# Kernel tuning notes

Measured on AMD Instinct MI355X. Metric: run time of the kernel, lower is better.

Reference implementation:

```python
import jax, jax.numpy as jnp
import numpy as np

D = 1024      # hidden_dim
E = 8         # num_experts
F = 512       # expert_dim


def setup_inputs() -> dict:
    key = jax.random.key(0)
    ks = jax.random.split(key, 7)
    B, N = 4, 4096
    s1 = 1.0 / np.sqrt(D)
    s2 = 1.0 / np.sqrt(F)
    return {
        "x": jax.random.normal(ks[0], (B, N, D), dtype=jnp.float32),
        "W1": jax.random.uniform(ks[1], (E, D, F), jnp.float32, -s1, s1),  # per-expert first linear
        "b1": jax.random.uniform(ks[2], (E, F), jnp.float32, -s1, s1),
        "W2": jax.random.uniform(ks[3], (E, F, D), jnp.float32, -s2, s2),  # per-expert second linear
        "b2": jax.random.uniform(ks[4], (E, D), jnp.float32, -s2, s2),
        "Wr": jax.random.uniform(ks[5], (D, E), jnp.float32, -s1, s1),    # router
        "br": jax.random.uniform(ks[6], (E,), jnp.float32, -s1, s1),
    }


def reference(x, W1, b1, W2, b2, Wr, br):
    # Router: softmax over experts per token. [B,N,E]
    router_weights = jax.nn.softmax(x @ Wr + br, axis=-1)
    # All experts on all tokens (dense soft-MoE), batched as grouped GEMMs.
    h = jax.nn.gelu(jnp.einsum('bnd,edf->bnef', x, W1) + b1, approximate=False)  # [B,N,E,F]
    y = jnp.einsum('bnef,efd->bned', h, W2) + b2[None, None]                      # [B,N,E,D]
    # Softmax-weighted combine over experts.
    return jnp.einsum('bned,bne->bnd', y, router_weights)
```

## Files before the change

### kernel.cpp

```cpp
#include <hip/hip_runtime.h>
#include <hip/hip_bf16.h>
#include <math.h>

#define MTOK 16384
#define DDIM 1024
#define EEXP 8
#define FDIM 512
#define EFK  4096

typedef __attribute__((ext_vector_type(8))) short short8;
typedef __attribute__((ext_vector_type(4))) float floatx4;

__device__ __forceinline__ void gld_lds16(const void* g, void* l) {
  __builtin_amdgcn_global_load_lds((const __attribute__((address_space(1))) void*)g,
                                   (__attribute__((address_space(3))) void*)l, 16, 0, 0);
}

__device__ __forceinline__ float gelu_fast(float v) {
  const float z  = v * 0.70710678118654752f;
  const float az = fabsf(z);
  const float t  = __builtin_amdgcn_rcpf(1.f + 0.3275911f * az);
  const float poly = t * (0.254829592f +
                     t * (-0.284496736f +
                     t * (1.421413741f +
                     t * (-1.453152027f +
                     t * 1.061405429f))));
  const float ex = __expf(-az * az);
  float erfv = 1.f - poly * ex;
  erfv = copysignf(erfv, z);
  return 0.5f * v * (1.f + erfv);
}

__global__ __launch_bounds__(256) void transpose_cast_kernel(
    const float* __restrict__ in, __hip_bfloat16* __restrict__ out, int R, int C) {
  __shared__ float tile[32][33];
  const float* inb = in + (size_t)blockIdx.z * R * C;
  __hip_bfloat16* outb = out + (size_t)blockIdx.z * R * C;
  const int c0 = blockIdx.x * 32, r0 = blockIdx.y * 32;
  const int tx = threadIdx.x & 31, ty = threadIdx.x >> 5;
#pragma unroll
  for (int i = 0; i < 4; ++i)
    tile[ty + i * 8][tx] = inb[(size_t)(r0 + ty + i * 8) * C + (c0 + tx)];
  __syncthreads();
#pragma unroll
  for (int i = 0; i < 4; ++i)
    outb[(size_t)(c0 + ty + i * 8) * R + (r0 + tx)] = __float2bfloat16(tile[tx][ty + i * 8]);
}

__global__ __launch_bounds__(256) void router_cast_kernel(
    const float* __restrict__ x, const float* __restrict__ Wr, const float* __restrict__ br,
    __hip_bfloat16* __restrict__ xbf, float* __restrict__ r) {
  const int wave = (blockIdx.x * 256 + threadIdx.x) >> 6;
  const int lane = threadIdx.x & 63;
  const float* xr = x + (size_t)wave * DDIM;
  float acc[EEXP];
#pragma unroll
  for (int e = 0; e < EEXP; ++e) acc[e] = 0.f;
#pragma unroll
  for (int i = 0; i < DDIM / 64; ++i) {
    const int d = i * 64 + lane;
    const float xv = xr[d];
    xbf[(size_t)wave * DDIM + d] = __float2bfloat16(xv);
    const float4* w4 = (const float4*)(Wr + (size_t)d * EEXP);
    const float4 w0 = w4[0], w1 = w4[1];
    acc[0] += xv * w0.x; acc[1] += xv * w0.y; acc[2] += xv * w0.z; acc[3] += xv * w0.w;
    acc[4] += xv * w1.x; acc[5] += xv * w1.y; acc[6] += xv * w1.z; acc[7] += xv * w1.w;
  }
#pragma unroll
  for (int off = 32; off; off >>= 1) {
#pragma unroll
    for (int e = 0; e < EEXP; ++e) acc[e] += __shfl_xor(acc[e], off, 64);
  }
  float mx = -1e30f;
#pragma unroll
  for (int e = 0; e < EEXP; ++e) { acc[e] += br[e]; mx = fmaxf(mx, acc[e]); }
  float s = 0.f;
#pragma unroll
  for (int e = 0; e < EEXP; ++e) { acc[e] = expf(acc[e] - mx); s += acc[e]; }
  const float inv = 1.f / s;
  if (lane < EEXP) r[(size_t)wave * EEXP + lane] = acc[lane] * inv;
}

#define BUFSZ 65536
#define AOFF  0
#define BOFF  32768

#define STAGE_A(Q1, QM, K0)                                                        \
  do {                                                                             \
    _Pragma("unroll") for (int r_ = 0; r_ < 2; ++r_) {                             \
      gld_lds16(gA + (size_t)(r_ * 128 + (QM) * 64 + wid * 8 + l3) * LDA_ +        \
                    (K0) + ((l7 ^ l3) * 8),                                        \
                ldsb + (Q1) * BUFSZ + AOFF + (QM) * 16384 +                        \
                    (r_ * 64 + wid * 8) * 128);                                    \
    }                                                                              \
  } while (0)

#define STAGE_B(Q1, QN, K0)                                                        \
  do {                                                                             \
    _Pragma("unroll") for (int r_ = 0; r_ < 2; ++r_) {                             \
      const int lin_ = r_ * 64 + wid * 8 + l3;                                     \
      gld_lds16(gB + (size_t)((lin_ >> 5) * 64 + (QN) * 32 + (lin_ & 31)) * LDB_ + \
                    (K0) + ((l7 ^ l3) * 8),                                        \
                ldsb + (Q1) * BUFSZ + BOFF + (QN) * 16384 +                        \
                    (r_ * 64 + wid * 8) * 128);                                    \
    }                                                                              \
  } while (0)

#define PHASE(P, QM, QN, VM, LA, LB, STAGE_STMT)                                   \
  do {                                                                             \
    asm volatile("s_waitcnt vmcnt(" VM ")\n\ts_barrier" ::: "memory");             \
    if (LA) {                                                                      \
      _Pragma("unroll") for (int i_ = 0; i_ < 4; ++i_)                             \
        _Pragma("unroll") for (int k_ = 0; k_ < 2; ++k_)                           \
          af[i_][k_] = *(const short8*)(ldsb + (P) * BUFSZ + AOFF +                \
              (QM) * 16384 + (wr * 64 + i_ * 16 + lanem) * 128 +                   \
              (((k_ * 4 + laneq) ^ swz) * 16));                                    \
    }                                                                              \
    if (LB) {                                                                      \
      _Pragma("unroll") for (int j_ = 0; j_ < 2; ++j_)                             \
        _Pragma("unroll") for (int k_ = 0; k_ < 2; ++k_)                           \
          bf[j_][k_] = *(const short8*)(ldsb + (P) * BUFSZ + BOFF +                \
              (QN) * 16384 + (wc * 32 + j_ * 16 + lanem) * 128 +                   \
              (((k_ * 4 + laneq) ^ swz) * 16));                                    \
    }                                                                              \
    STAGE_STMT;                                                                    \
    __builtin_amdgcn_s_setprio(1);                                                 \
    _Pragma("unroll") for (int i_ = 0; i_ < 4; ++i_)                               \
      _Pragma("unroll") for (int j_ = 0; j_ < 2; ++j_)                             \
        _Pragma("unroll") for (int k_ = 0; k_ < 2; ++k_)                           \
          acc[(QM) * 4 + i_][(QN) * 2 + j_] =                                      \
              __builtin_amdgcn_mfma_f32_16x16x32_bf16(                             \
                  af[i_][k_], bf[j_][k_], acc[(QM) * 4 + i_][(QN) * 2 + j_],       \
                  0, 0, 0);                                                        \
    __builtin_amdgcn_s_setprio(0);                                                 \
  } while (0)

#define GEMM_CORE(NT)                                                              \
  STAGE_A(0, 0, 0);                                                                \
  STAGE_B(0, 0, 0);                                                                \
  STAGE_B(0, 1, 0);                                                                \
  STAGE_A(0, 1, 0);                                                                \
  for (int kt = 0; kt < (NT) - 1; ++kt) {                                          \
    const int p_ = kt & 1, q_ = p_ ^ 1, k1_ = (kt + 1) * 64;                       \
    PHASE(p_, 0, 0, "4", 1, 1, STAGE_A(q_, 0, k1_));                               \
    PHASE(p_, 0, 1, "4", 0, 1, STAGE_B(q_, 0, k1_));                               \
    PHASE(p_, 1, 1, "4", 1, 0, STAGE_B(q_, 1, k1_));                               \
    PHASE(p_, 1, 0, "6", 0, 1, STAGE_A(q_, 1, k1_));                               \
  }                                                                                \
  {                                                                                \
    const int p_ = ((NT) - 1) & 1;                                                 \
    PHASE(p_, 0, 0, "4", 1, 1, (void)0);                                           \
    PHASE(p_, 0, 1, "2", 0, 1, (void)0);                                           \
    PHASE(p_, 1, 1, "0", 1, 0, (void)0);                                           \
    PHASE(p_, 1, 0, "0", 0, 1, (void)0);                                           \
  }

__global__ __launch_bounds__(512, 2) void gemm_h_kernel(
    const __hip_bfloat16* __restrict__ A, const __hip_bfloat16* __restrict__ W1t,
    const float* __restrict__ b1, const float* __restrict__ r,
    __hip_bfloat16* __restrict__ Hs) {
  const int bid = blockIdx.x;
  const int strip = bid & 63, fb = (bid >> 6) & 1, e = bid >> 7;
  const int T0 = strip * 256, F0 = fb * 256;

  __shared__ char ldsb[2 * BUFSZ];

  const int tid = threadIdx.x, lane = tid & 63, wid = tid >> 6;
  const int wr = wid >> 2, wc = wid & 3;
  const int lanem = lane & 15, laneq = lane >> 4;
  const int l3 = lane >> 3, l7 = lane & 7;
  const int swz = lanem & 7;
  const int LDA_ = DDIM, LDB_ = DDIM;

  const __hip_bfloat16* gA = W1t + (size_t)e * FDIM * DDIM + (size_t)F0 * DDIM;
  const __hip_bfloat16* gB = A + (size_t)T0 * DDIM;

  floatx4 acc[8][4];
#pragma unroll
  for (int i = 0; i < 8; ++i)
#pragma unroll
    for (int j = 0; j < 4; ++j) acc[i][j] = (floatx4){0.f, 0.f, 0.f, 0.f};
  short8 af[4][2], bf[2][2];

  GEMM_CORE(DDIM / 64);

#pragma unroll
  for (int nj = 0; nj < 4; ++nj) {
    const int tok = T0 + wc * 64 + nj * 16 + lanem;
    const float rv = r[(size_t)tok * EEXP + e];
#pragma unroll
    for (int mi = 0; mi < 8; ++mi) {
      const int f = F0 + wr * 128 + mi * 16 + laneq * 4;
      const float4 b4 = *(const float4*)(b1 + e * FDIM + f);
      union { ushort4 u; __hip_bfloat16 h[4]; } pk;
      pk.h[0] = __float2bfloat16(gelu_fast(acc[mi][nj][0] + b4.x) * rv);
      pk.h[1] = __float2bfloat16(gelu_fast(acc[mi][nj][1] + b4.y) * rv);
      pk.h[2] = __float2bfloat16(gelu_fast(acc[mi][nj][2] + b4.z) * rv);
      pk.h[3] = __float2bfloat16(gelu_fast(acc[mi][nj][3] + b4.w) * rv);
      *(ushort4*)(Hs + (size_t)tok * EFK + e * FDIM + f) = pk.u;
    }
  }
}

__global__ __launch_bounds__(512, 2) void gemm_out_kernel(
    const __hip_bfloat16* __restrict__ Hs, const __hip_bfloat16* __restrict__ W2t,
    const float* __restrict__ b2, const float* __restrict__ r,
    float* __restrict__ out) {
  const int bid = blockIdx.x;
  const int strip = (bid >> 5) * 8 + (bid & 7);
  const int dq = (bid >> 3) & 3;
  const int T0 = strip * 256, D0 = dq * 256;

  __shared__ char ldsb[2 * BUFSZ];

  const int tid = threadIdx.x, lane = tid & 63, wid = tid >> 6;
  const int wr = wid >> 2, wc = wid & 3;
  const int lanem = lane & 15, laneq = lane >> 4;
  const int l3 = lane >> 3, l7 = lane & 7;
  const int swz = lanem & 7;
  const int LDA_ = EFK, LDB_ = EFK;

  const __hip_bfloat16* gA = W2t + (size_t)D0 * EFK;
  const __hip_bfloat16* gB = Hs + (size_t)T0 * EFK;

  floatx4 acc[8][4];
#pragma unroll
  for (int i = 0; i < 8; ++i)
#pragma unroll
    for (int j = 0; j < 4; ++j) acc[i][j] = (floatx4){0.f, 0.f, 0.f, 0.f};
  short8 af[4][2], bf[2][2];

  GEMM_CORE(EFK / 64);

#pragma unroll
  for (int mi = 0; mi < 8; ++mi) {
    const int d0 = D0 + wr * 128 + mi * 16 + laneq * 4;
    float4 b2v[EEXP];
#pragma unroll
    for (int e = 0; e < EEXP; ++e) b2v[e] = *(const float4*)(b2 + e * DDIM + d0);
#pragma unroll
    for (int nj = 0; nj < 4; ++nj) {
      const int tok = T0 + wc * 64 + nj * 16 + lanem;
      const float4* r4 = (const float4*)(r + (size_t)tok * EEXP);
      const float4 r0 = r4[0], r1 = r4[1];
      const float rv[EEXP] = {r0.x, r0.y, r0.z, r0.w, r1.x, r1.y, r1.z, r1.w};
      float bx = 0.f, by = 0.f, bz = 0.f, bw = 0.f;
#pragma unroll
      for (int e = 0; e < EEXP; ++e) {
        bx += rv[e] * b2v[e].x; by += rv[e] * b2v[e].y;
        bz += rv[e] * b2v[e].z; bw += rv[e] * b2v[e].w;
      }
      float4 o;
      o.x = acc[mi][nj][0] + bx; o.y = acc[mi][nj][1] + by;
      o.z = acc[mi][nj][2] + bz; o.w = acc[mi][nj][3] + bw;
      *(float4*)(out + (size_t)tok * DDIM + d0) = o;
    }
  }
}

extern "C" void kernel_launch(void* const* d_in, const int* in_sizes, int n_in,
                              void* d_out, int out_size, void* d_ws, size_t ws_size,
                              hipStream_t stream) {
  const float* x  = (const float*)d_in[0];
  const float* W1 = (const float*)d_in[1];
  const float* b1 = (const float*)d_in[2];
  const float* W2 = (const float*)d_in[3];
  const float* b2 = (const float*)d_in[4];
  const float* Wr = (const float*)d_in[5];
  const float* br = (const float*)d_in[6];
  float* out = (float*)d_out;

  char* ws = (char*)d_ws;
  __hip_bfloat16* xbf = (__hip_bfloat16*)(ws);
  __hip_bfloat16* W1t = (__hip_bfloat16*)(ws + (32u << 20));
  __hip_bfloat16* W2t = (__hip_bfloat16*)(ws + (40u << 20));
  float*          r   = (float*)(ws + (48u << 20));
  __hip_bfloat16* Hs  = (__hip_bfloat16*)(ws + (48u << 20) + (1u << 19));

  transpose_cast_kernel<<<dim3(FDIM / 32, DDIM / 32, EEXP), 256, 0, stream>>>(W1, W1t, DDIM, FDIM);
  transpose_cast_kernel<<<dim3(DDIM / 32, EFK / 32, 1), 256, 0, stream>>>(W2, W2t, EFK, DDIM);
  router_cast_kernel<<<MTOK / 4, 256, 0, stream>>>(x, Wr, br, xbf, r);
  gemm_h_kernel<<<dim3((MTOK / 256) * (FDIM / 256) * EEXP), 512, 0, stream>>>(xbf, W1t, b1, r, Hs);
  gemm_out_kernel<<<dim3((MTOK / 256) * (DDIM / 256)), 512, 0, stream>>>(Hs, W2t, b2, r, out);
}
```

Measured before the change: 480.8 us.

## Restructure GEMM phase pipeline: barrier after staging, two barriers per phase, reorder MFMA loop

Each phase of the double-buffered GEMM main loop now issues its LDS fragment reads and the next global->LDS stage before waiting on vmcnt and the workgroup barrier. It then waits for lgkmcnt(0) and adds a trailing barrier after the MFMA block, with sched_barriers fencing the compiler schedule. This is meant to overlap LDS reads and global loads with the wait and keep waves in lockstep across MFMA clusters. The MFMA loop order is also changed to iterate k outermost. The cost is two barriers per phase instead of one, and the vmcnt accounting has been recomputed, which risks races if the counts are wrong.

```diff
diff --git a/kernel.cpp b/kernel.cpp
--- a/kernel.cpp
+++ b/kernel.cpp
@@ -106,9 +106,13 @@
     }                                                                              \
   } while (0)
 
-#define PHASE(P, QM, QN, VM, LA, LB, STAGE_STMT)                                   \
+#define VM4    asm volatile("s_waitcnt vmcnt(4)" ::: "memory")
+#define VM2    asm volatile("s_waitcnt vmcnt(2)" ::: "memory")
+#define VM0    asm volatile("s_waitcnt vmcnt(0)" ::: "memory")
+#define VMNONE ((void)0)
+
+#define PHASE(P, QM, QN, LA, LB, STAGE_STMT, VMWAIT)                               \
   do {                                                                             \
-    asm volatile("s_waitcnt vmcnt(" VM ")\n\ts_barrier" ::: "memory");             \
     if (LA) {                                                                      \
       _Pragma("unroll") for (int i_ = 0; i_ < 4; ++i_)                             \
         _Pragma("unroll") for (int k_ = 0; k_ < 2; ++k_)                           \
@@ -124,15 +128,21 @@
               (((k_ * 4 + laneq) ^ swz) * 16));                                    \
     }                                                                              \
     STAGE_STMT;                                                                    \
+    __builtin_amdgcn_sched_barrier(0);                                             \
+    VMWAIT;                                                                        \
+    __builtin_amdgcn_s_barrier();                                                  \
+    asm volatile("s_waitcnt lgkmcnt(0)" ::: "memory");                             \
+    __builtin_amdgcn_sched_barrier(0);                                             \
     __builtin_amdgcn_s_setprio(1);                                                 \
-    _Pragma("unroll") for (int i_ = 0; i_ < 4; ++i_)                               \
-      _Pragma("unroll") for (int j_ = 0; j_ < 2; ++j_)                             \
-        _Pragma("unroll") for (int k_ = 0; k_ < 2; ++k_)                           \
+    _Pragma("unroll") for (int k_ = 0; k_ < 2; ++k_)                               \
+      _Pragma("unroll") for (int i_ = 0; i_ < 4; ++i_)                             \
+        _Pragma("unroll") for (int j_ = 0; j_ < 2; ++j_)                           \
           acc[(QM) * 4 + i_][(QN) * 2 + j_] =                                      \
               __builtin_amdgcn_mfma_f32_16x16x32_bf16(                             \
                   af[i_][k_], bf[j_][k_], acc[(QM) * 4 + i_][(QN) * 2 + j_],       \
                   0, 0, 0);                                                        \
     __builtin_amdgcn_s_setprio(0);                                                 \
+    __builtin_amdgcn_s_barrier();                                                  \
   } while (0)
 
 #define GEMM_CORE(NT)                                                              \
@@ -140,19 +150,21 @@
   STAGE_B(0, 0, 0);                                                                \
   STAGE_B(0, 1, 0);                                                                \
   STAGE_A(0, 1, 0);                                                                \
+  VM4;                                                                             \
+  __builtin_amdgcn_s_barrier();                                                    \
   for (int kt = 0; kt < (NT) - 1; ++kt) {                                          \
     const int p_ = kt & 1, q_ = p_ ^ 1, k1_ = (kt + 1) * 64;                       \
-    PHASE(p_, 0, 0, "4", 1, 1, STAGE_A(q_, 0, k1_));                               \
-    PHASE(p_, 0, 1, "4", 0, 1, STAGE_B(q_, 0, k1_));                               \
-    PHASE(p_, 1, 1, "4", 1, 0, STAGE_B(q_, 1, k1_));                               \
-    PHASE(p_, 1, 0, "6", 0, 1, STAGE_A(q_, 1, k1_));                               \
+    PHASE(p_, 0, 0, 1, 1, STAGE_A(q_, 0, k1_), VM4);                               \
+    PHASE(p_, 0, 1, 0, 1, STAGE_B(q_, 0, k1_), VM4);                               \
+    PHASE(p_, 1, 1, 1, 0, STAGE_B(q_, 1, k1_), VMNONE);                            \
+    PHASE(p_, 1, 0, 0, 1, STAGE_A(q_, 1, k1_), VM4);                               \
   }                                                                                \
   {                                                                                \
     const int p_ = ((NT) - 1) & 1;                                                 \
-    PHASE(p_, 0, 0, "4", 1, 1, (void)0);                                           \
-    PHASE(p_, 0, 1, "2", 0, 1, (void)0);                                           \
-    PHASE(p_, 1, 1, "0", 1, 0, (void)0);                                           \
-    PHASE(p_, 1, 0, "0", 0, 1, (void)0);                                           \
+    PHASE(p_, 0, 0, 1, 1, (void)0, VM2);                                           \
+    PHASE(p_, 0, 1, 0, 1, (void)0, VM0);                                           \
+    PHASE(p_, 1, 1, 1, 0, (void)0, VMNONE);                                        \
+    PHASE(p_, 1, 0, 0, 1, (void)0, VMNONE);                                        \
   }
 
 __global__ __launch_bounds__(512, 2) void gemm_h_kernel(
```

Result: no change. 489.8 us (+1.9%).

## Restructure GEMM main loop to one barrier per k-tile with batched LDS reads

Applied to the files above, without the earlier changes.

Replaces the four-phase per-k-tile schedule (four barriers, interleaved partial stage issues and fragment reloads) with one bulk prefetch of the next tile, all A/B fragments loaded from LDS up front, and MFMA quadrants gated by staged lgkmcnt waits. A single vmcnt(0)+barrier closes each iteration. This cuts barrier count and lets LDS reads overlap MFMAs, but adds register pressure (af doubled, bf doubled) under launch_bounds(512,2). It also waits for all global loads at the end of each tile, so global latency is hidden only by one tile of compute.

```diff
diff --git a/kernel.cpp b/kernel.cpp
--- a/kernel.cpp
+++ b/kernel.cpp
@@ -106,53 +106,62 @@
     }                                                                              \
   } while (0)
 
-#define PHASE(P, QM, QN, VM, LA, LB, STAGE_STMT)                                   \
-  do {                                                                             \
-    asm volatile("s_waitcnt vmcnt(" VM ")\n\ts_barrier" ::: "memory");             \
-    if (LA) {                                                                      \
-      _Pragma("unroll") for (int i_ = 0; i_ < 4; ++i_)                             \
-        _Pragma("unroll") for (int k_ = 0; k_ < 2; ++k_)                           \
-          af[i_][k_] = *(const short8*)(ldsb + (P) * BUFSZ + AOFF +                \
-              (QM) * 16384 + (wr * 64 + i_ * 16 + lanem) * 128 +                   \
-              (((k_ * 4 + laneq) ^ swz) * 16));                                    \
-    }                                                                              \
-    if (LB) {                                                                      \
-      _Pragma("unroll") for (int j_ = 0; j_ < 2; ++j_)                             \
-        _Pragma("unroll") for (int k_ = 0; k_ < 2; ++k_)                           \
-          bf[j_][k_] = *(const short8*)(ldsb + (P) * BUFSZ + BOFF +                \
-              (QN) * 16384 + (wc * 32 + j_ * 16 + lanem) * 128 +                   \
-              (((k_ * 4 + laneq) ^ swz) * 16));                                    \
-    }                                                                              \
-    STAGE_STMT;                                                                    \
-    __builtin_amdgcn_s_setprio(1);                                                 \
+#define STAGE_ALL(Q1, K0)                                                          \
+  do { STAGE_A(Q1, 0, K0); STAGE_B(Q1, 0, K0); STAGE_B(Q1, 1, K0);                 \
+       STAGE_A(Q1, 1, K0); } while (0)
+
+#define READS_A(P, QM)                                                             \
+  _Pragma("unroll") for (int i_ = 0; i_ < 4; ++i_)                                 \
+    _Pragma("unroll") for (int k_ = 0; k_ < 2; ++k_)                               \
+      af[QM][i_][k_] = *(const short8*)(ldsb + (P) * BUFSZ + AOFF +                \
+          (QM) * 16384 + (wr * 64 + i_ * 16 + lanem) * 128 +                       \
+          (((k_ * 4 + laneq) ^ swz) * 16));
+
+#define READS_B(P)                                                                 \
+  _Pragma("unroll") for (int n_ = 0; n_ < 4; ++n_)                                 \
+    _Pragma("unroll") for (int k_ = 0; k_ < 2; ++k_)                               \
+      bf[n_][k_] = *(const short8*)(ldsb + (P) * BUFSZ + BOFF +                    \
+          (n_ >> 1) * 16384 + (wc * 32 + (n_ & 1) * 16 + lanem) * 128 +            \
+          (((k_ * 4 + laneq) ^ swz) * 16));
+
+#define MFMA_Q(QM, QN)                                                             \
+  _Pragma("unroll") for (int k_ = 0; k_ < 2; ++k_)                                 \
     _Pragma("unroll") for (int i_ = 0; i_ < 4; ++i_)                               \
       _Pragma("unroll") for (int j_ = 0; j_ < 2; ++j_)                             \
-        _Pragma("unroll") for (int k_ = 0; k_ < 2; ++k_)                           \
-          acc[(QM) * 4 + i_][(QN) * 2 + j_] =                                      \
-              __builtin_amdgcn_mfma_f32_16x16x32_bf16(                             \
-                  af[i_][k_], bf[j_][k_], acc[(QM) * 4 + i_][(QN) * 2 + j_],       \
-                  0, 0, 0);                                                        \
+        acc[(QM) * 4 + i_][(QN) * 2 + j_] =                                        \
+            __builtin_amdgcn_mfma_f32_16x16x32_bf16(                               \
+                af[QM][i_][k_], bf[(QN) * 2 + j_][k_],                             \
+                acc[(QM) * 4 + i_][(QN) * 2 + j_], 0, 0, 0);
+
+#define LGKM(N)                                                                    \
+  asm volatile("s_waitcnt lgkmcnt(" #N ")" ::: "memory");                          \
+  __builtin_amdgcn_sched_barrier(0)
+
+#define GEMM_CORE(NT)                                                              \
+  STAGE_ALL(0, 0);                                                                 \
+  asm volatile("s_waitcnt vmcnt(0)\n\ts_barrier" ::: "memory");                    \
+  for (int kt = 0; kt < (NT); ++kt) {                                              \
+    const int p_ = kt & 1;                                                         \
+    if (kt + 1 < (NT)) STAGE_ALL(p_ ^ 1, (kt + 1) * 64);                           \
+    READS_A(p_, 0);                                                                \
+    READS_B(p_);                                                                   \
+    __builtin_amdgcn_sched_barrier(0);                                             \
+    READS_A(p_, 1);                                                                \
+    __builtin_amdgcn_sched_barrier(0);                                             \
+    LGKM(12);                                                                      \
+    __builtin_amdgcn_s_setprio(1);                                                 \
+    MFMA_Q(0, 0);                                                                  \
     __builtin_amdgcn_s_setprio(0);                                                 \
-  } while (0)
-
-#define GEMM_CORE(NT)                                                              \
-  STAGE_A(0, 0, 0);                                                                \
-  STAGE_B(0, 0, 0);                                                                \
-  STAGE_B(0, 1, 0);                                                                \
-  STAGE_A(0, 1, 0);                                                                \
-  for (int kt = 0; kt < (NT) - 1; ++kt) {                                          \
-    const int p_ = kt & 1, q_ = p_ ^ 1, k1_ = (kt + 1) * 64;                       \
-    PHASE(p_, 0, 0, "4", 1, 1, STAGE_A(q_, 0, k1_));                               \
-    PHASE(p_, 0, 1, "4", 0, 1, STAGE_B(q_, 0, k1_));                               \
-    PHASE(p_, 1, 1, "4", 1, 0, STAGE_B(q_, 1, k1_));                               \
-    PHASE(p_, 1, 0, "6", 0, 1, STAGE_A(q_, 1, k1_));                               \
-  }                                                                                \
-  {                                                                                \
-    const int p_ = ((NT) - 1) & 1;                                                 \
-    PHASE(p_, 0, 0, "4", 1, 1, (void)0);                                           \
-    PHASE(p_, 0, 1, "2", 0, 1, (void)0);                                           \
-    PHASE(p_, 1, 1, "0", 1, 0, (void)0);                                           \
-    PHASE(p_, 1, 0, "0", 0, 1, (void)0);                                           \
+    LGKM(8);                                                                       \
+    __builtin_amdgcn_s_setprio(1);                                                 \
+    MFMA_Q(0, 1);                                                                  \
+    __builtin_amdgcn_s_setprio(0);                                                 \
+    LGKM(0);                                                                       \
+    __builtin_amdgcn_s_setprio(1);                                                 \
+    MFMA_Q(1, 1);                                                                  \
+    MFMA_Q(1, 0);                                                                  \
+    __builtin_amdgcn_s_setprio(0);                                                 \
+    asm volatile("s_waitcnt vmcnt(0)\n\ts_barrier" ::: "memory");                  \
   }
 
 __global__ __launch_bounds__(512, 2) void gemm_h_kernel(
@@ -180,7 +189,7 @@
   for (int i = 0; i < 8; ++i)
 #pragma unroll
     for (int j = 0; j < 4; ++j) acc[i][j] = (floatx4){0.f, 0.f, 0.f, 0.f};
-  short8 af[4][2], bf[2][2];
+  short8 af[2][4][2], bf[4][2];
 
   GEMM_CORE(DDIM / 64);
 
@@ -228,7 +237,7 @@
   for (int i = 0; i < 8; ++i)
 #pragma unroll
     for (int j = 0; j < 4; ++j) acc[i][j] = (floatx4){0.f, 0.f, 0.f, 0.f};
-  short8 af[4][2], bf[2][2];
+  short8 af[2][4][2], bf[4][2];
 
   GEMM_CORE(EFK / 64);
 
```

New measurement: 470.1 us. 1.02x faster.

## Shrink GEMM tiles to 128x256xK32 with triple-buffered LDS pipeline

Applied to the files above, without the earlier changes.

Both grouped GEMM kernels drop from 256x256 tiles with K=64 double buffering to 128x256 tiles with K=32 and a three-stage LDS ring. Each thread now issues one direct-to-LDS load per operand chunk, using a new XOR swizzle. Launch bounds rise to 4 blocks per CU and the block-to-XCD mapping is changed. The aim is higher occupancy and better latency hiding, at the cost of less data reuse per tile and more barriers per K step.

```diff
diff --git a/kernel.cpp b/kernel.cpp
--- a/kernel.cpp
+++ b/kernel.cpp
@@ -81,116 +81,101 @@
   if (lane < EEXP) r[(size_t)wave * EEXP + lane] = acc[lane] * inv;
 }
 
-#define BUFSZ 65536
-#define AOFF  0
-#define BOFF  32768
-
-#define STAGE_A(Q1, QM, K0)                                                        \
-  do {                                                                             \
-    _Pragma("unroll") for (int r_ = 0; r_ < 2; ++r_) {                             \
-      gld_lds16(gA + (size_t)(r_ * 128 + (QM) * 64 + wid * 8 + l3) * LDA_ +        \
-                    (K0) + ((l7 ^ l3) * 8),                                        \
-                ldsb + (Q1) * BUFSZ + AOFF + (QM) * 16384 +                        \
-                    (r_ * 64 + wid * 8) * 128);                                    \
-    }                                                                              \
+#define BUFB  24576
+#define BOFFB 8192
+
+#define STAGE3(O2, K0)                                                          \
+  do {                                                                          \
+    gld_lds16(pA  + (K0), ldsb + (O2) + (tid << 4));                            \
+    gld_lds16(pB0 + (K0), ldsb + (O2) + 8192  + (tid << 4));                    \
+    gld_lds16(pB1 + (K0), ldsb + (O2) + 16384 + (tid << 4));                    \
   } while (0)
 
-#define STAGE_B(Q1, QN, K0)                                                        \
-  do {                                                                             \
-    _Pragma("unroll") for (int r_ = 0; r_ < 2; ++r_) {                             \
-      const int lin_ = r_ * 64 + wid * 8 + l3;                                     \
-      gld_lds16(gB + (size_t)((lin_ >> 5) * 64 + (QN) * 32 + (lin_ & 31)) * LDB_ + \
-                    (K0) + ((l7 ^ l3) * 8),                                        \
-                ldsb + (Q1) * BUFSZ + BOFF + (QN) * 16384 +                        \
-                    (r_ * 64 + wid * 8) * 128);                                    \
-    }                                                                              \
-  } while (0)
-
-#define PHASE(P, QM, QN, VM, LA, LB, STAGE_STMT)                                   \
-  do {                                                                             \
-    asm volatile("s_waitcnt vmcnt(" VM ")\n\ts_barrier" ::: "memory");             \
-    if (LA) {                                                                      \
-      _Pragma("unroll") for (int i_ = 0; i_ < 4; ++i_)                             \
-        _Pragma("unroll") for (int k_ = 0; k_ < 2; ++k_)                           \
-          af[i_][k_] = *(const short8*)(ldsb + (P) * BUFSZ + AOFF +                \
-              (QM) * 16384 + (wr * 64 + i_ * 16 + lanem) * 128 +                   \
-              (((k_ * 4 + laneq) ^ swz) * 16));                                    \
-    }                                                                              \
-    if (LB) {                                                                      \
-      _Pragma("unroll") for (int j_ = 0; j_ < 2; ++j_)                             \
-        _Pragma("unroll") for (int k_ = 0; k_ < 2; ++k_)                           \
-          bf[j_][k_] = *(const short8*)(ldsb + (P) * BUFSZ + BOFF +                \
-              (QN) * 16384 + (wc * 32 + j_ * 16 + lanem) * 128 +                   \
-              (((k_ * 4 + laneq) ^ swz) * 16));                                    \
-    }                                                                              \
-    STAGE_STMT;                                                                    \
-    __builtin_amdgcn_s_setprio(1);                                                 \
-    _Pragma("unroll") for (int i_ = 0; i_ < 4; ++i_)                               \
-      _Pragma("unroll") for (int j_ = 0; j_ < 2; ++j_)                             \
-        _Pragma("unroll") for (int k_ = 0; k_ < 2; ++k_)                           \
-          acc[(QM) * 4 + i_][(QN) * 2 + j_] =                                      \
-              __builtin_amdgcn_mfma_f32_16x16x32_bf16(                             \
-                  af[i_][k_], bf[j_][k_], acc[(QM) * 4 + i_][(QN) * 2 + j_],       \
-                  0, 0, 0);                                                        \
-    __builtin_amdgcn_s_setprio(0);                                                 \
-  } while (0)
-
-#define GEMM_CORE(NT)                                                              \
-  STAGE_A(0, 0, 0);                                                                \
-  STAGE_B(0, 0, 0);                                                                \
-  STAGE_B(0, 1, 0);                                                                \
-  STAGE_A(0, 1, 0);                                                                \
-  for (int kt = 0; kt < (NT) - 1; ++kt) {                                          \
-    const int p_ = kt & 1, q_ = p_ ^ 1, k1_ = (kt + 1) * 64;                       \
-    PHASE(p_, 0, 0, "4", 1, 1, STAGE_A(q_, 0, k1_));                               \
-    PHASE(p_, 0, 1, "4", 0, 1, STAGE_B(q_, 0, k1_));                               \
-    PHASE(p_, 1, 1, "4", 1, 0, STAGE_B(q_, 1, k1_));                               \
-    PHASE(p_, 1, 0, "6", 0, 1, STAGE_A(q_, 1, k1_));                               \
-  }                                                                                \
-  {                                                                                \
-    const int p_ = ((NT) - 1) & 1;                                                 \
-    PHASE(p_, 0, 0, "4", 1, 1, (void)0);                                           \
-    PHASE(p_, 0, 1, "2", 0, 1, (void)0);                                           \
-    PHASE(p_, 1, 1, "0", 1, 0, (void)0);                                           \
-    PHASE(p_, 1, 0, "0", 0, 1, (void)0);                                           \
-  }
-
-__global__ __launch_bounds__(512, 2) void gemm_h_kernel(
+#define READS8(O0)                                                              \
+  _Pragma("unroll") for (int i_ = 0; i_ < 4; ++i_)                              \
+    af[i_] = *(const short8*)(ldsb + (O0) + laneA + i_ * 1024);                 \
+  _Pragma("unroll") for (int j_ = 0; j_ < 4; ++j_)                              \
+    bf[j_] = *(const short8*)(ldsb + (O0) + laneB + j_ * 1024);
+
+#define MFMA16                                                                  \
+  _Pragma("unroll") for (int i_ = 0; i_ < 4; ++i_)                              \
+    _Pragma("unroll") for (int j_ = 0; j_ < 4; ++j_)                            \
+      acc[i_][j_] = __builtin_amdgcn_mfma_f32_16x16x32_bf16(                    \
+          af[i_], bf[j_], acc[i_][j_], 0, 0, 0);
+
+#define GEMM_CORE(NT)                                                           \
+  STAGE3(0, 0);                                                                 \
+  STAGE3(BUFB, 32);                                                             \
+  asm volatile("s_waitcnt vmcnt(3)\n\ts_barrier" ::: "memory");                 \
+  {                                                                             \
+    int o0 = 0, o1 = BUFB, o2 = 2 * BUFB;                                       \
+    for (int kt = 0; kt < (NT) - 2; ++kt) {                                     \
+      READS8(o0);                                                               \
+      STAGE3(o2, (kt + 2) * 32);                                                \
+      __builtin_amdgcn_s_setprio(1);                                            \
+      MFMA16;                                                                   \
+      __builtin_amdgcn_s_setprio(0);                                            \
+      __builtin_amdgcn_sched_barrier(0);                                        \
+      asm volatile("s_waitcnt vmcnt(3)\n\ts_barrier" ::: "memory");             \
+      const int t_ = o0; o0 = o1; o1 = o2; o2 = t_;                             \
+    }                                                                           \
+    READS8(o0);                                                                 \
+    __builtin_amdgcn_s_setprio(1);                                              \
+    MFMA16;                                                                     \
+    __builtin_amdgcn_s_setprio(0);                                              \
+    __builtin_amdgcn_sched_barrier(0);                                          \
+    asm volatile("s_waitcnt vmcnt(0)\n\ts_barrier" ::: "memory");               \
+    READS8(o1);                                                                 \
+    __builtin_amdgcn_s_setprio(1);                                              \
+    MFMA16;                                                                     \
+    __builtin_amdgcn_s_setprio(0);                                              \
+  }
+
+#define STAGE_PTR(gbase, LD, posv)                                              \
+  ((gbase) + (size_t)(2 * ((posv) >> 3) + ((((posv) & 7) ^ (((posv) >> 3) & 7)) >> 2)) * (LD) \
+           + ((((posv) & 7) ^ (((posv) >> 3) & 7)) & 3) * 8)
+
+__global__ __launch_bounds__(512, 4) void gemm_h_kernel(
     const __hip_bfloat16* __restrict__ A, const __hip_bfloat16* __restrict__ W1t,
     const float* __restrict__ b1, const float* __restrict__ r,
     __hip_bfloat16* __restrict__ Hs) {
   const int bid = blockIdx.x;
-  const int strip = bid & 63, fb = (bid >> 6) & 1, e = bid >> 7;
-  const int T0 = strip * 256, F0 = fb * 256;
-
-  __shared__ char ldsb[2 * BUFSZ];
+  const int xcd = bid & 7, t = bid >> 3;
+  const int strip = (t >> 5) * 8 + xcd;
+  const int em = t & 31, e = em >> 2, mb = em & 3;
+  const int T0 = strip * 256, F0 = mb * 128;
+
+  __shared__ char ldsb[3 * BUFB];
 
   const int tid = threadIdx.x, lane = tid & 63, wid = tid >> 6;
   const int wr = wid >> 2, wc = wid & 3;
   const int lanem = lane & 15, laneq = lane >> 4;
-  const int l3 = lane >> 3, l7 = lane & 7;
-  const int swz = lanem & 7;
-  const int LDA_ = DDIM, LDB_ = DDIM;
+  const int cswz = (((lanem & 1) << 2) | laneq) ^ (lanem >> 1);
+  const int laneA = (lanem >> 1) * 128 + cswz * 16 + wr * 4096;
+  const int laneB = BOFFB + (lanem >> 1) * 128 + cswz * 16 + wc * 4096;
 
   const __hip_bfloat16* gA = W1t + (size_t)e * FDIM * DDIM + (size_t)F0 * DDIM;
   const __hip_bfloat16* gB = A + (size_t)T0 * DDIM;
-
-  floatx4 acc[8][4];
-#pragma unroll
-  for (int i = 0; i < 8; ++i)
+  const __hip_bfloat16* pA  = STAGE_PTR(gA, DDIM, tid);
+  const __hip_bfloat16* pB0 = STAGE_PTR(gB, DDIM, tid);
+  const __hip_bfloat16* pB1 = STAGE_PTR(gB, DDIM, tid + 512);
+
+  floatx4 acc[4][4];
+#pragma unroll
+  for (int i = 0; i < 4; ++i)
 #pragma unroll
     for (int j = 0; j < 4; ++j) acc[i][j] = (floatx4){0.f, 0.f, 0.f, 0.f};
-  short8 af[4][2], bf[2][2];
-
-  GEMM_CORE(DDIM / 64);
+  short8 af[4], bf[4];
+
+  GEMM_CORE(DDIM / 32);
 
 #pragma unroll
   for (int nj = 0; nj < 4; ++nj) {
     const int tok = T0 + wc * 64 + nj * 16 + lanem;
     const float rv = r[(size_t)tok * EEXP + e];
 #pragma unroll
-    for (int mi = 0; mi < 8; ++mi) {
-      const int f = F0 + wr * 128 + mi * 16 + laneq * 4;
+    for (int mi = 0; mi < 4; ++mi) {
+      const int f = F0 + wr * 64 + mi * 16 + laneq * 4;
       const float4 b4 = *(const float4*)(b1 + e * FDIM + f);
       union { ushort4 u; __hip_bfloat16 h[4]; } pk;
       pk.h[0] = __float2bfloat16(gelu_fast(acc[mi][nj][0] + b4.x) * rv);
@@ -202,39 +187,43 @@
   }
 }
 
-__global__ __launch_bounds__(512, 2) void gemm_out_kernel(
+__global__ __launch_bounds__(512, 4) void gemm_out_kernel(
     const __hip_bfloat16* __restrict__ Hs, const __hip_bfloat16* __restrict__ W2t,
     const float* __restrict__ b2, const float* __restrict__ r,
     float* __restrict__ out) {
   const int bid = blockIdx.x;
-  const int strip = (bid >> 5) * 8 + (bid & 7);
-  const int dq = (bid >> 3) & 3;
-  const int T0 = strip * 256, D0 = dq * 256;
-
-  __shared__ char ldsb[2 * BUFSZ];
+  const int xcd = bid & 7, t = bid >> 3;
+  const int strip = (t >> 3) * 8 + xcd;
+  const int mb = t & 7;
+  const int T0 = strip * 256, D0 = mb * 128;
+
+  __shared__ char ldsb[3 * BUFB];
 
   const int tid = threadIdx.x, lane = tid & 63, wid = tid >> 6;
   const int wr = wid >> 2, wc = wid & 3;
   const int lanem = lane & 15, laneq = lane >> 4;
-  const int l3 = lane >> 3, l7 = lane & 7;
-  const int swz = lanem & 7;
-  const int LDA_ = EFK, LDB_ = EFK;
+  const int cswz = (((lanem & 1) << 2) | laneq) ^ (lanem >> 1);
+  const int laneA = (lanem >> 1) * 128 + cswz * 16 + wr * 4096;
+  const int laneB = BOFFB + (lanem >> 1) * 128 + cswz * 16 + wc * 4096;
 
   const __hip_bfloat16* gA = W2t + (size_t)D0 * EFK;
   const __hip_bfloat16* gB = Hs + (size_t)T0 * EFK;
-
-  floatx4 acc[8][4];
-#pragma unroll
-  for (int i = 0; i < 8; ++i)
+  const __hip_bfloat16* pA  = STAGE_PTR(gA, EFK, tid);
+  const __hip_bfloat16* pB0 = STAGE_PTR(gB, EFK, tid);
+  const __hip_bfloat16* pB1 = STAGE_PTR(gB, EFK, tid + 512);
+
+  floatx4 acc[4][4];
+#pragma unroll
+  for (int i = 0; i < 4; ++i)
 #pragma unroll
     for (int j = 0; j < 4; ++j) acc[i][j] = (floatx4){0.f, 0.f, 0.f, 0.f};
-  short8 af[4][2], bf[2][2];
-
-  GEMM_CORE(EFK / 64);
-
-#pragma unroll
-  for (int mi = 0; mi < 8; ++mi) {
-    const int d0 = D0 + wr * 128 + mi * 16 + laneq * 4;
+  short8 af[4], bf[4];
+
+  GEMM_CORE(EFK / 32);
+
+#pragma unroll
+  for (int mi = 0; mi < 4; ++mi) {
+    const int d0 = D0 + wr * 64 + mi * 16 + laneq * 4;
     float4 b2v[EEXP];
 #pragma unroll
     for (int e = 0; e < EEXP; ++e) b2v[e] = *(const float4*)(b2 + e * DDIM + d0);
@@ -280,6 +269,6 @@
   transpose_cast_kernel<<<dim3(FDIM / 32, DDIM / 32, EEXP), 256, 0, stream>>>(W1, W1t, DDIM, FDIM);
   transpose_cast_kernel<<<dim3(DDIM / 32, EFK / 32, 1), 256, 0, stream>>>(W2, W2t, EFK, DDIM);
   router_cast_kernel<<<MTOK / 4, 256, 0, stream>>>(x, Wr, br, xbf, r);
-  gemm_h_kernel<<<dim3((MTOK / 256) * (FDIM / 256) * EEXP), 512, 0, stream>>>(xbf, W1t, b1, r, Hs);
-  gemm_out_kernel<<<dim3((MTOK / 256) * (DDIM / 256)), 512, 0, stream>>>(Hs, W2t, b2, r, out);
-}
+  gemm_h_kernel<<<dim3((MTOK / 256) * (FDIM / 128) * EEXP), 512, 0, stream>>>(xbf, W1t, b1, r, Hs);
+  gemm_out_kernel<<<dim3((MTOK / 256) * (DDIM / 128)), 512, 0, stream>>>(Hs, W2t, b2, r, out);
+}
```

Measured after the change: 512.6 us. +6.6%, slower.
